# Kernel optimization log

Measured on AMD Instinct MI355X. Metric: run time of the kernel, lower is better.

The kernel has to match this reference:

```python
import jax, jax.numpy as jnp
import numpy as np

K = 3
P = K // 2


def _conv(x, w, b):
    y = jax.lax.conv_general_dilated(x, w, (1, 1), [(P, P), (P, P)],
                                     dimension_numbers=('NCHW', 'OIHW', 'NCHW'))
    return y + b[None, :, None, None]


def _deform_sample(x, py, px):
    # x: [B,C,H,W]; py,px: [B,KK,H,W] float sample coords -> [B,C,KK,H,W]
    B, C, H, W = x.shape
    xf = x.reshape(B, C, H * W)
    y0 = jnp.floor(py)
    x0 = jnp.floor(px)
    wy = py - y0
    wx = px - x0

    def corner(yi, xi, w):
        valid = (yi >= 0) & (yi < H) & (xi >= 0) & (xi < W)  # zero-pad outside
        idx = (jnp.clip(yi, 0, H - 1) * W + jnp.clip(xi, 0, W - 1)).astype(jnp.int32)
        g = jax.vmap(lambda xb, ib: xb[:, ib])(xf, idx)  # [B,C,KK,H,W]
        return g * (w * valid)[:, None]

    return (corner(y0, x0, (1 - wy) * (1 - wx)) + corner(y0, x0 + 1, (1 - wy) * wx)
            + corner(y0 + 1, x0, wy * (1 - wx)) + corner(y0 + 1, x0 + 1, wy * wx))


def setup_inputs() -> dict:
    key = jax.random.key(0)
    ks = jax.random.split(key, 8)
    B, C, H, W = 4, 256, 80, 80
    x = jax.random.normal(ks[0], (B, C, H, W), dtype=jnp.float32)
    offset_w = jax.random.normal(ks[1], (2 * K * K, C, K, K), dtype=jnp.float32) * 0.01
    offset_b = jax.random.normal(ks[2], (2 * K * K,), dtype=jnp.float32) * 0.01
    dcn_w = jax.random.normal(ks[3], (C, C, K, K), dtype=jnp.float32) * (1.0 / np.sqrt(C * K * K))
    gamma = jnp.ones((C,), jnp.float32)
    beta = jnp.zeros((C,), jnp.float32)
    mean = jax.random.normal(ks[4], (C,), dtype=jnp.float32) * 0.1
    var = jax.random.uniform(ks[5], (C,), dtype=jnp.float32, minval=0.5, maxval=1.5)
    return {'x': x, 'offset_w': offset_w, 'offset_b': offset_b, 'dcn_w': dcn_w,
            'gamma': gamma, 'beta': beta, 'mean': mean, 'var': var}


def reference(x, offset_w, offset_b, dcn_w, gamma, beta, mean, var):
    B, C, H, W = x.shape
    # offset conv -> [B, KK, 2(dy,dx), H, W] (torchvision DeformConv2d layout)
    off = _conv(x, offset_w, offset_b).reshape(B, K * K, 2, H, W)
    ki = jnp.repeat(jnp.arange(K), K).astype(x.dtype)  # kernel-tap row offset
    kj = jnp.tile(jnp.arange(K), K).astype(x.dtype)    # kernel-tap col offset
    hh = jnp.arange(H, dtype=x.dtype)
    ww = jnp.arange(W, dtype=x.dtype)
    py = off[:, :, 0] + (hh - P)[None, None, :, None] + ki[None, :, None, None]
    px = off[:, :, 1] + (ww - P)[None, None, None, :] + kj[None, :, None, None]
    vals = _deform_sample(x, py, px)                      # [B,C,KK,H,W]
    y = jnp.einsum('bckhw,ock->bohw', vals, dcn_w.reshape(C, C, K * K))
    # eval-mode BatchNorm + SiLU
    inv = jax.lax.rsqrt(var + 1e-5)
    y = (y - mean[None, :, None, None]) * (gamma * inv)[None, :, None, None] + beta[None, :, None, None]
    y = y * jax.nn.sigmoid(y)
    return x + y
```

## Files before the change

kernel.cpp:

```cpp
#include <hip/hip_runtime.h>
#include <math.h>
#include <stdint.h>

#define BATCH 4
#define CH    256
#define HH    80
#define WW    80
#define HW    (HH*WW)
#define NPIX  (BATCH*HW)
#define KK    9
#define CO    18
#define NCHUNK 72
#define NIV   36
#define PXB   64
#define NBLK  (NPIX/PXB)
#define AST   72

typedef _Float16 half8 __attribute__((ext_vector_type(8)));
typedef float    f32x4 __attribute__((ext_vector_type(4)));

__global__ __launch_bounds__(256) void k_transpose_x(const float* __restrict__ x,
                                                     _Float16* __restrict__ xt) {
    __shared__ float tile[32][33];
    int b  = blockIdx.z;
    int c0 = blockIdx.y * 32;
    int p0 = blockIdx.x * 32;
    int tx = threadIdx.x;
    int ty = threadIdx.y;
    const float* xb = x + (size_t)b * CH * HW;
    #pragma unroll
    for (int i = 0; i < 32; i += 8)
        tile[ty + i][tx] = xb[(size_t)(c0 + ty + i) * HW + p0 + tx];
    __syncthreads();
    _Float16* xtb = xt + (size_t)b * HW * CH;
    #pragma unroll
    for (int i = 0; i < 32; i += 8)
        xtb[(size_t)(p0 + ty + i) * CH + c0 + tx] = (_Float16)tile[tx][ty + i];
}

__global__ __launch_bounds__(256) void k_pack_all(const float* __restrict__ w,
                                                  const float* __restrict__ ow,
                                                  _Float16* __restrict__ wp,
                                                  _Float16* __restrict__ wpo) {
    int idx = blockIdx.x * 256 + threadIdx.x;
    if (idx < NIV * 16384) {
        int e    = idx & 7;
        int lane = (idx >> 3) & 63;
        int nn   = (idx >> 9) & 1;
        int ks   = (idx >> 10) & 1;
        int og   = (idx >> 11) & 7;
        int iv   = idx >> 14;
        int oc = og * 32 + nn * 16 + (lane & 15);
        int kl = ks * 32 + (lane >> 4) * 8 + e;
        int kg = iv * 64 + kl;
        int q  = kg >> 5;
        int tap = q >> 3;
        int c   = (q & 7) * 32 + (kg & 31);
        wp[idx] = (_Float16)w[((size_t)oc * CH + c) * KK + tap];
        return;
    }
    int idx2 = idx - NIV * 16384;
    if (idx2 >= NCHUNK * 1024) return;
    int e    = idx2 & 7;
    int lane = (idx2 >> 3) & 63;
    int nf   = (idx2 >> 9) & 1;
    int q    = idx2 >> 10;
    int oc  = nf * 16 + (lane & 15);
    int kic = (lane >> 4) * 8 + e;
    int tap = q >> 3;
    int c   = (q & 7) * 32 + kic;
    float v = (oc < CO) ? ow[((size_t)oc * CH + c) * KK + tap] : 0.f;
    wpo[idx2] = (_Float16)v;
}

__global__ __launch_bounds__(256) void k_offset(const _Float16* __restrict__ xt,
                                                const _Float16* __restrict__ wopf,
                                                float* __restrict__ off4) {
    int t = threadIdx.x, lane = t & 63, wvi = t >> 6;
    int lm = lane & 15, kg8 = (lane >> 4) * 8;
    int ksl = blockIdx.y;
    int pixbase = blockIdx.x * 64;
    int bb = pixbase / HW;
    int apx = pixbase % HW + wvi * 16 + lm;
    int h = apx / WW, w = apx % WW;
    const _Float16* xtb = xt + (size_t)bb * HW * CH;
    f32x4 acc0 = (f32x4)0.f, acc1 = (f32x4)0.f;
    #pragma unroll
    for (int qq = 0; qq < 18; ++qq) {
        int q = ksl * 18 + qq;
        int tap = q >> 3, cg = q & 7;
        int ki = tap / 3, kj = tap % 3;
        int yy = h + ki - 1, xx = w + kj - 1;
        bool ok = (yy >= 0) && (yy < HH) && (xx >= 0) && (xx < WW);
        int yc = min(max(yy, 0), HH - 1), xc = min(max(xx, 0), WW - 1);
        half8 a = {0, 0, 0, 0, 0, 0, 0, 0};
        if (ok) a = *(const half8*)(xtb + (size_t)(yc * WW + xc) * CH + cg * 32 + kg8);
        const _Float16* wb = wopf + (size_t)q * 1024 + lane * 8;
        half8 b0 = *(const half8*)(wb);
        half8 b1 = *(const half8*)(wb + 512);
        acc0 = __builtin_amdgcn_mfma_f32_16x16x32_f16(a, b0, acc0, 0, 0, 0);
        acc1 = __builtin_amdgcn_mfma_f32_16x16x32_f16(a, b1, acc1, 0, 0, 0);
    }
    float* op = off4 + (size_t)ksl * NPIX * CO;
    int prow = (lane >> 4) * 4;
    #pragma unroll
    for (int r = 0; r < 4; ++r) {
        int pix = pixbase + wvi * 16 + prow + r;
        op[(size_t)pix * CO + lm] = acc0[r];
        if (lm < CO - 16) op[(size_t)pix * CO + 16 + lm] = acc1[r];
    }
}

#define BODY(IV, BCUR, BNXT, RBUF, WBUF)                                           \
  {                                                                                \
    __syncthreads();                                                               \
    const int iv_ = (IV);                                                          \
    half8 pre[4]; float cwa[4];                                                    \
    if (iv_ < NIV - 1) {                                                           \
      const _Float16* wb = wpk4 + (size_t)(iv_ + 1) * 16384 + og * 2048 + lane * 8;\
      BNXT[0] = *(const half8*)(wb);                                               \
      BNXT[1] = *(const half8*)(wb + 512);                                         \
      BNXT[2] = *(const half8*)(wb + 1024);                                        \
      BNXT[3] = *(const half8*)(wb + 1536);                                        \
      int chunk = 2 * (iv_ + 1) + sub;                                             \
      int tap = chunk >> 3, cg = chunk & 7;                                        \
      int4 ncb = cbl[gpx][tap]; float4 ncw = cwl[gpx][tap];                        \
      pre[0] = *(const half8*)(xtb + (size_t)ncb.x + cg * 32 + ko);                \
      pre[1] = *(const half8*)(xtb + (size_t)ncb.y + cg * 32 + ko);                \
      pre[2] = *(const half8*)(xtb + (size_t)ncb.z + cg * 32 + ko);                \
      pre[3] = *(const half8*)(xtb + (size_t)ncb.w + cg * 32 + ko);                \
      cwa[0] = ncw.x; cwa[1] = ncw.y; cwa[2] = ncw.z; cwa[3] = ncw.w;              \
    }                                                                              \
    __builtin_amdgcn_s_setprio(1);                                                 \
    _Pragma("unroll")                                                              \
    for (int mm = 0; mm < 4; ++mm) {                                               \
      half8 a0 = *(const half8*)&Ab[RBUF][(mm * 16 + lm) * AST + kg8];             \
      half8 a1 = *(const half8*)&Ab[RBUF][(mm * 16 + lm) * AST + 32 + kg8];        \
      acc[mm][0] = __builtin_amdgcn_mfma_f32_16x16x32_f16(a0, BCUR[0], acc[mm][0], 0, 0, 0); \
      acc[mm][1] = __builtin_amdgcn_mfma_f32_16x16x32_f16(a0, BCUR[1], acc[mm][1], 0, 0, 0); \
      acc[mm][0] = __builtin_amdgcn_mfma_f32_16x16x32_f16(a1, BCUR[2], acc[mm][0], 0, 0, 0); \
      acc[mm][1] = __builtin_amdgcn_mfma_f32_16x16x32_f16(a1, BCUR[3], acc[mm][1], 0, 0, 0); \
    }                                                                              \
    __builtin_amdgcn_s_setprio(0);                                                 \
    if (iv_ < NIV - 1) {                                                           \
      half8 v = pre[0] * (_Float16)cwa[0];                                         \
      v += pre[1] * (_Float16)cwa[1];                                              \
      v += pre[2] * (_Float16)cwa[2];                                              \
      v += pre[3] * (_Float16)cwa[3];                                              \
      *(half8*)&Ab[WBUF][gpx * AST + cq * 8] = v;                                  \
    }                                                                              \
  }

__global__ __launch_bounds__(512, 4) void k_main(const float* __restrict__ x,
                                                 const _Float16* __restrict__ xt,
                                                 const _Float16* __restrict__ wpk4,
                                                 const float* __restrict__ off4,
                                                 const float* __restrict__ obias,
                                                 const float* __restrict__ gamma,
                                                 const float* __restrict__ beta,
                                                 const float* __restrict__ mean,
                                                 const float* __restrict__ var,
                                                 float* __restrict__ out) {
    __shared__ _Float16 Ab[2][PXB * AST];
    __shared__ int4     cbl[PXB][KK];
    __shared__ float4   cwl[PXB][KK];

    int t = threadIdx.x, lane = t & 63, og = t >> 6;
    int lm = lane & 15, kg8 = (lane >> 4) * 8;
    int tile = ((int)blockIdx.x & 7) * (NBLK / 8) + ((int)blockIdx.x >> 3);
    int pixbase = tile * PXB;
    int bb = pixbase / HW, hw0 = pixbase % HW;
    const _Float16* xtb = xt + (size_t)bb * HW * CH;

    for (int task = t; task < PXB * KK; task += 512) {
        int p = task / KK, tap = task - (task / KK) * KK;
        int pix = pixbase + p;
        float dy = obias[2 * tap], dx = obias[2 * tap + 1];
        #pragma unroll
        for (int ks = 0; ks < 4; ++ks) {
            dy += off4[(size_t)ks * NPIX * CO + (size_t)pix * CO + 2 * tap];
            dx += off4[(size_t)ks * NPIX * CO + (size_t)pix * CO + 2 * tap + 1];
        }
        int hw = pix % HW, hc = hw / WW, wc = hw % WW;
        int ki = tap / 3, kj = tap % 3;
        float py = dy + (float)(hc - 1 + ki);
        float px = dx + (float)(wc - 1 + kj);
        float y0f = floorf(py), x0f = floorf(px);
        float wy = py - y0f, wx = px - x0f;
        int y0 = (int)y0f, x0 = (int)x0f;
        int cb[4]; float cw[4];
        #pragma unroll
        for (int cy = 0; cy < 2; ++cy)
            #pragma unroll
            for (int cx = 0; cx < 2; ++cx) {
                int yy = y0 + cy, xx = x0 + cx;
                bool okc = (yy >= 0) && (yy < HH) && (xx >= 0) && (xx < WW);
                int yc = min(max(yy, 0), HH - 1);
                int xc = min(max(xx, 0), WW - 1);
                float wgt = (cy ? wy : 1.f - wy) * (cx ? wx : 1.f - wx);
                cb[cy * 2 + cx] = (yc * WW + xc) * CH;
                cw[cy * 2 + cx] = okc ? wgt : 0.f;
            }
        cbl[p][tap] = make_int4(cb[0], cb[1], cb[2], cb[3]);
        cwl[p][tap] = make_float4(cw[0], cw[1], cw[2], cw[3]);
    }
    __syncthreads();

    int gpx = t >> 3, cq = t & 7;
    int sub = cq >> 2, ko = (cq & 3) * 8;

    half8 bfA[4], bfB[4];
    {
        const _Float16* wb = wpk4 + og * 2048 + lane * 8;
        bfA[0] = *(const half8*)(wb);
        bfA[1] = *(const half8*)(wb + 512);
        bfA[2] = *(const half8*)(wb + 1024);
        bfA[3] = *(const half8*)(wb + 1536);
    }
    {
        int4 cb = cbl[gpx][0];
        float4 cw = cwl[gpx][0];
        int cg = sub;
        half8 v = *(const half8*)(xtb + (size_t)cb.x + cg * 32 + ko) * (_Float16)cw.x;
        v += *(const half8*)(xtb + (size_t)cb.y + cg * 32 + ko) * (_Float16)cw.y;
        v += *(const half8*)(xtb + (size_t)cb.z + cg * 32 + ko) * (_Float16)cw.z;
        v += *(const half8*)(xtb + (size_t)cb.w + cg * 32 + ko) * (_Float16)cw.w;
        *(half8*)&Ab[0][gpx * AST + cq * 8] = v;
    }

    f32x4 acc[4][2];
    #pragma unroll
    for (int mm = 0; mm < 4; ++mm) {
        acc[mm][0] = (f32x4)0.f;
        acc[mm][1] = (f32x4)0.f;
    }

    for (int ii = 0; ii < NIV; ii += 2) {
        BODY(ii,     bfA, bfB, 0, 1)
        BODY(ii + 1, bfB, bfA, 1, 0)
    }

    const float* xb2  = x   + (size_t)bb * CH * HW;
    float*       outb = out + (size_t)bb * CH * HW;
    #pragma unroll
    for (int nn = 0; nn < 2; ++nn) {
        int oc = og * 32 + nn * 16 + lm;
        float sc = gamma[oc] * rsqrtf(var[oc] + 1e-5f);
        float mn = mean[oc], bt = beta[oc];
        const float* xr   = xb2  + (size_t)oc * HW + hw0;
        float*       orow = outb + (size_t)oc * HW + hw0;
        #pragma unroll
        for (int mm = 0; mm < 4; ++mm) {
            int pb2 = mm * 16 + (lane >> 4) * 4;
            #pragma unroll
            for (int r = 0; r < 4; ++r) {
                float yv = (acc[mm][nn][r] - mn) * sc + bt;
                float s = yv * __builtin_amdgcn_rcpf(1.f + __expf(-yv));
                orow[pb2 + r] = xr[pb2 + r] + s;
            }
        }
    }
}

extern "C" void kernel_launch(void* const* d_in, const int* in_sizes, int n_in,
                              void* d_out, int out_size, void* d_ws, size_t ws_size,
                              hipStream_t stream) {
    const float* x        = (const float*)d_in[0];
    const float* offset_w = (const float*)d_in[1];
    const float* offset_b = (const float*)d_in[2];
    const float* dcn_w    = (const float*)d_in[3];
    const float* gamma    = (const float*)d_in[4];
    const float* beta     = (const float*)d_in[5];
    const float* mean     = (const float*)d_in[6];
    const float* var      = (const float*)d_in[7];
    float* out = (float*)d_out;

    _Float16* xt   = (_Float16*)d_ws;
    _Float16* wpk4 = xt + (size_t)NPIX * CH;
    _Float16* wopf = wpk4 + (size_t)NIV * 16384;
    float*    off4 = (float*)(wopf + (size_t)NCHUNK * 1024);

    k_transpose_x<<<dim3(HW / 32, CH / 32, BATCH), dim3(32, 8), 0, stream>>>(x, xt);
    k_pack_all<<<(NIV * 16384 + NCHUNK * 1024 + 255) / 256, 256, 0, stream>>>(dcn_w, offset_w, wpk4, wopf);
    k_offset<<<dim3(NBLK, 4), 256, 0, stream>>>(xt, wopf, off4);
    k_main<<<NBLK, 512, 0, stream>>>(x, xt, wpk4, off4, offset_b,
                                     gamma, beta, mean, var, out);
}
```

Baseline: 96.41 us.

## Split main GEMM reduction across two K-slices with fp16 partials and finish kernel

Splits the deformable GEMM's reduction dimension into two halves, run as separate blocks (grid y=2), so the launch has twice as many blocks and better fills the GPU. Each half writes fp16 partial sums to workspace, and a new elementwise kernel adds the halves and applies BatchNorm, SiLU and the residual. If the workspace is too small it falls back to the original fused kernel. The cost is an extra launch, extra global traffic for the partials and reduced precision from storing partials in fp16. Corner weights are now also computed twice, once per slice.

Measured after the change: 348.4 us. 261% more time.

```diff
diff --git a/kernel.cpp b/kernel.cpp
--- a/kernel.cpp
+++ b/kernel.cpp
@@ -17,6 +17,7 @@
 #define AST   72
 
 typedef _Float16 half8 __attribute__((ext_vector_type(8)));
+typedef _Float16 half4 __attribute__((ext_vector_type(4)));
 typedef float    f32x4 __attribute__((ext_vector_type(4)));
 
 __global__ __launch_bounds__(256) void k_transpose_x(const float* __restrict__ x,
@@ -111,68 +112,11 @@
     }
 }
 
-#define BODY(IV, BCUR, BNXT, RBUF, WBUF)                                           \
-  {                                                                                \
-    __syncthreads();                                                               \
-    const int iv_ = (IV);                                                          \
-    half8 pre[4]; float cwa[4];                                                    \
-    if (iv_ < NIV - 1) {                                                           \
-      const _Float16* wb = wpk4 + (size_t)(iv_ + 1) * 16384 + og * 2048 + lane * 8;\
-      BNXT[0] = *(const half8*)(wb);                                               \
-      BNXT[1] = *(const half8*)(wb + 512);                                         \
-      BNXT[2] = *(const half8*)(wb + 1024);                                        \
-      BNXT[3] = *(const half8*)(wb + 1536);                                        \
-      int chunk = 2 * (iv_ + 1) + sub;                                             \
-      int tap = chunk >> 3, cg = chunk & 7;                                        \
-      int4 ncb = cbl[gpx][tap]; float4 ncw = cwl[gpx][tap];                        \
-      pre[0] = *(const half8*)(xtb + (size_t)ncb.x + cg * 32 + ko);                \
-      pre[1] = *(const half8*)(xtb + (size_t)ncb.y + cg * 32 + ko);                \
-      pre[2] = *(const half8*)(xtb + (size_t)ncb.z + cg * 32 + ko);                \
-      pre[3] = *(const half8*)(xtb + (size_t)ncb.w + cg * 32 + ko);                \
-      cwa[0] = ncw.x; cwa[1] = ncw.y; cwa[2] = ncw.z; cwa[3] = ncw.w;              \
-    }                                                                              \
-    __builtin_amdgcn_s_setprio(1);                                                 \
-    _Pragma("unroll")                                                              \
-    for (int mm = 0; mm < 4; ++mm) {                                               \
-      half8 a0 = *(const half8*)&Ab[RBUF][(mm * 16 + lm) * AST + kg8];             \
-      half8 a1 = *(const half8*)&Ab[RBUF][(mm * 16 + lm) * AST + 32 + kg8];        \
-      acc[mm][0] = __builtin_amdgcn_mfma_f32_16x16x32_f16(a0, BCUR[0], acc[mm][0], 0, 0, 0); \
-      acc[mm][1] = __builtin_amdgcn_mfma_f32_16x16x32_f16(a0, BCUR[1], acc[mm][1], 0, 0, 0); \
-      acc[mm][0] = __builtin_amdgcn_mfma_f32_16x16x32_f16(a1, BCUR[2], acc[mm][0], 0, 0, 0); \
-      acc[mm][1] = __builtin_amdgcn_mfma_f32_16x16x32_f16(a1, BCUR[3], acc[mm][1], 0, 0, 0); \
-    }                                                                              \
-    __builtin_amdgcn_s_setprio(0);                                                 \
-    if (iv_ < NIV - 1) {                                                           \
-      half8 v = pre[0] * (_Float16)cwa[0];                                         \
-      v += pre[1] * (_Float16)cwa[1];                                              \
-      v += pre[2] * (_Float16)cwa[2];                                              \
-      v += pre[3] * (_Float16)cwa[3];                                              \
-      *(half8*)&Ab[WBUF][gpx * AST + cq * 8] = v;                                  \
-    }                                                                              \
-  }
-
-__global__ __launch_bounds__(512, 4) void k_main(const float* __restrict__ x,
-                                                 const _Float16* __restrict__ xt,
-                                                 const _Float16* __restrict__ wpk4,
-                                                 const float* __restrict__ off4,
-                                                 const float* __restrict__ obias,
-                                                 const float* __restrict__ gamma,
-                                                 const float* __restrict__ beta,
-                                                 const float* __restrict__ mean,
-                                                 const float* __restrict__ var,
-                                                 float* __restrict__ out) {
-    __shared__ _Float16 Ab[2][PXB * AST];
-    __shared__ int4     cbl[PXB][KK];
-    __shared__ float4   cwl[PXB][KK];
-
-    int t = threadIdx.x, lane = t & 63, og = t >> 6;
-    int lm = lane & 15, kg8 = (lane >> 4) * 8;
-    int tile = ((int)blockIdx.x & 7) * (NBLK / 8) + ((int)blockIdx.x >> 3);
-    int pixbase = tile * PXB;
-    int bb = pixbase / HW, hw0 = pixbase % HW;
-    const _Float16* xtb = xt + (size_t)bb * HW * CH;
-
-    for (int task = t; task < PXB * KK; task += 512) {
+__device__ __forceinline__ void build_corners(int t, int nthr, int pixbase,
+                                              const float* __restrict__ off4,
+                                              const float* __restrict__ obias,
+                                              int4 (*cbl)[KK], float4 (*cwl)[KK]) {
+    for (int task = t; task < PXB * KK; task += nthr) {
         int p = task / KK, tap = task - (task / KK) * KK;
         int pix = pixbase + p;
         float dy = obias[2 * tap], dx = obias[2 * tap + 1];
@@ -204,6 +148,171 @@
         cbl[p][tap] = make_int4(cb[0], cb[1], cb[2], cb[3]);
         cwl[p][tap] = make_float4(cw[0], cw[1], cw[2], cw[3]);
     }
+}
+
+#define BODY(IV, IVEND, BCUR, BNXT, RBUF, WBUF)                                    \
+  {                                                                                \
+    __syncthreads();                                                               \
+    const int iv_ = (IV);                                                          \
+    half8 pre[4]; float cwa[4];                                                    \
+    if (iv_ < (IVEND) - 1) {                                                       \
+      const _Float16* wb = wpk4 + (size_t)(iv_ + 1) * 16384 + og * 2048 + lane * 8;\
+      BNXT[0] = *(const half8*)(wb);                                               \
+      BNXT[1] = *(const half8*)(wb + 512);                                         \
+      BNXT[2] = *(const half8*)(wb + 1024);                                        \
+      BNXT[3] = *(const half8*)(wb + 1536);                                        \
+      int chunk = 2 * (iv_ + 1) + sub;                                             \
+      int tap = chunk >> 3, cg = chunk & 7;                                        \
+      int4 ncb = cbl[gpx][tap]; float4 ncw = cwl[gpx][tap];                        \
+      pre[0] = *(const half8*)(xtb + (size_t)ncb.x + cg * 32 + ko);                \
+      pre[1] = *(const half8*)(xtb + (size_t)ncb.y + cg * 32 + ko);                \
+      pre[2] = *(const half8*)(xtb + (size_t)ncb.z + cg * 32 + ko);                \
+      pre[3] = *(const half8*)(xtb + (size_t)ncb.w + cg * 32 + ko);                \
+      cwa[0] = ncw.x; cwa[1] = ncw.y; cwa[2] = ncw.z; cwa[3] = ncw.w;              \
+    }                                                                              \
+    __builtin_amdgcn_s_setprio(1);                                                 \
+    _Pragma("unroll")                                                              \
+    for (int mm = 0; mm < 4; ++mm) {                                               \
+      half8 a0 = *(const half8*)&Ab[RBUF][(mm * 16 + lm) * AST + kg8];             \
+      half8 a1 = *(const half8*)&Ab[RBUF][(mm * 16 + lm) * AST + 32 + kg8];        \
+      acc[mm][0] = __builtin_amdgcn_mfma_f32_16x16x32_f16(a0, BCUR[0], acc[mm][0], 0, 0, 0); \
+      acc[mm][1] = __builtin_amdgcn_mfma_f32_16x16x32_f16(a0, BCUR[1], acc[mm][1], 0, 0, 0); \
+      acc[mm][0] = __builtin_amdgcn_mfma_f32_16x16x32_f16(a1, BCUR[2], acc[mm][0], 0, 0, 0); \
+      acc[mm][1] = __builtin_amdgcn_mfma_f32_16x16x32_f16(a1, BCUR[3], acc[mm][1], 0, 0, 0); \
+    }                                                                              \
+    __builtin_amdgcn_s_setprio(0);                                                 \
+    if (iv_ < (IVEND) - 1) {                                                       \
+      half8 v = pre[0] * (_Float16)cwa[0];                                         \
+      v += pre[1] * (_Float16)cwa[1];                                              \
+      v += pre[2] * (_Float16)cwa[2];                                              \
+      v += pre[3] * (_Float16)cwa[3];                                              \
+      *(half8*)&Ab[WBUF][gpx * AST + cq * 8] = v;                                  \
+    }                                                                              \
+  }
+
+__global__ __launch_bounds__(512, 6) void k_main_sk(const _Float16* __restrict__ xt,
+                                                    const _Float16* __restrict__ wpk4,
+                                                    const float* __restrict__ off4,
+                                                    const float* __restrict__ obias,
+                                                    _Float16* __restrict__ P) {
+    __shared__ _Float16 Ab[2][PXB * AST];
+    __shared__ int4     cbl[PXB][KK];
+    __shared__ float4   cwl[PXB][KK];
+
+    int t = threadIdx.x, lane = t & 63, og = t >> 6;
+    int lm = lane & 15, kg8 = (lane >> 4) * 8;
+    int ksl = blockIdx.y;
+    int iv0 = ksl * (NIV / 2);
+    int tile = ((int)blockIdx.x & 7) * (NBLK / 8) + ((int)blockIdx.x >> 3);
+    int pixbase = tile * PXB;
+    int bb = pixbase / HW, hw0 = pixbase % HW;
+    const _Float16* xtb = xt + (size_t)bb * HW * CH;
+
+    build_corners(t, 512, pixbase, off4, obias, cbl, cwl);
+    __syncthreads();
+
+    int gpx = t >> 3, cq = t & 7;
+    int sub = cq >> 2, ko = (cq & 3) * 8;
+
+    half8 bfA[4], bfB[4];
+    {
+        const _Float16* wb = wpk4 + (size_t)iv0 * 16384 + og * 2048 + lane * 8;
+        bfA[0] = *(const half8*)(wb);
+        bfA[1] = *(const half8*)(wb + 512);
+        bfA[2] = *(const half8*)(wb + 1024);
+        bfA[3] = *(const half8*)(wb + 1536);
+    }
+    {
+        int chunk0 = 2 * iv0 + sub;
+        int tap0 = chunk0 >> 3, cg0 = chunk0 & 7;
+        int4 cb = cbl[gpx][tap0];
+        float4 cw = cwl[gpx][tap0];
+        half8 v = *(const half8*)(xtb + (size_t)cb.x + cg0 * 32 + ko) * (_Float16)cw.x;
+        v += *(const half8*)(xtb + (size_t)cb.y + cg0 * 32 + ko) * (_Float16)cw.y;
+        v += *(const half8*)(xtb + (size_t)cb.z + cg0 * 32 + ko) * (_Float16)cw.z;
+        v += *(const half8*)(xtb + (size_t)cb.w + cg0 * 32 + ko) * (_Float16)cw.w;
+        *(half8*)&Ab[0][gpx * AST + cq * 8] = v;
+    }
+
+    f32x4 acc[4][2];
+    #pragma unroll
+    for (int mm = 0; mm < 4; ++mm) {
+        acc[mm][0] = (f32x4)0.f;
+        acc[mm][1] = (f32x4)0.f;
+    }
+
+    int ivend = iv0 + NIV / 2;
+    for (int ii = iv0; ii < ivend; ii += 2) {
+        BODY(ii,     ivend, bfA, bfB, 0, 1)
+        BODY(ii + 1, ivend, bfB, bfA, 1, 0)
+    }
+
+    _Float16* Pb = P + (size_t)ksl * NPIX * CH + (size_t)bb * CH * HW;
+    #pragma unroll
+    for (int nn = 0; nn < 2; ++nn) {
+        int oc = og * 32 + nn * 16 + lm;
+        _Float16* prow = Pb + (size_t)oc * HW + hw0;
+        #pragma unroll
+        for (int mm = 0; mm < 4; ++mm) {
+            int pb2 = mm * 16 + (lane >> 4) * 4;
+            half4 h = {(_Float16)acc[mm][nn][0], (_Float16)acc[mm][nn][1],
+                       (_Float16)acc[mm][nn][2], (_Float16)acc[mm][nn][3]};
+            *(half4*)&prow[pb2] = h;
+        }
+    }
+}
+
+__global__ __launch_bounds__(512) void k_finish(const _Float16* __restrict__ P,
+                                                const float* __restrict__ x,
+                                                const float* __restrict__ gamma,
+                                                const float* __restrict__ beta,
+                                                const float* __restrict__ mean,
+                                                const float* __restrict__ var,
+                                                float* __restrict__ out) {
+    int tid = blockIdx.x * 512 + threadIdx.x;
+    size_t base = (size_t)tid * 8;
+    int oc = (tid / (HW / 8)) & (CH - 1);
+    half8 p0 = *(const half8*)(P + base);
+    half8 p1 = *(const half8*)(P + (size_t)NPIX * CH + base);
+    float sc = gamma[oc] * rsqrtf(var[oc] + 1e-5f);
+    float mn = mean[oc], bt = beta[oc];
+    float4 x0 = *(const float4*)(x + base);
+    float4 x1 = *(const float4*)(x + base + 4);
+    float o[8];
+    #pragma unroll
+    for (int j = 0; j < 8; ++j) {
+        float y = (float)p0[j] + (float)p1[j];
+        float yv = (y - mn) * sc + bt;
+        float s = yv * __builtin_amdgcn_rcpf(1.f + __expf(-yv));
+        float xv = (j < 4) ? ((const float*)&x0)[j] : ((const float*)&x1)[j - 4];
+        o[j] = xv + s;
+    }
+    *(float4*)(out + base)     = make_float4(o[0], o[1], o[2], o[3]);
+    *(float4*)(out + base + 4) = make_float4(o[4], o[5], o[6], o[7]);
+}
+
+__global__ __launch_bounds__(512, 4) void k_main_fused(const float* __restrict__ x,
+                                                       const _Float16* __restrict__ xt,
+                                                       const _Float16* __restrict__ wpk4,
+                                                       const float* __restrict__ off4,
+                                                       const float* __restrict__ obias,
+                                                       const float* __restrict__ gamma,
+                                                       const float* __restrict__ beta,
+                                                       const float* __restrict__ mean,
+                                                       const float* __restrict__ var,
+                                                       float* __restrict__ out) {
+    __shared__ _Float16 Ab[2][PXB * AST];
+    __shared__ int4     cbl[PXB][KK];
+    __shared__ float4   cwl[PXB][KK];
+
+    int t = threadIdx.x, lane = t & 63, og = t >> 6;
+    int lm = lane & 15, kg8 = (lane >> 4) * 8;
+    int tile = ((int)blockIdx.x & 7) * (NBLK / 8) + ((int)blockIdx.x >> 3);
+    int pixbase = tile * PXB;
+    int bb = pixbase / HW, hw0 = pixbase % HW;
+    const _Float16* xtb = xt + (size_t)bb * HW * CH;
+
+    build_corners(t, 512, pixbase, off4, obias, cbl, cwl);
     __syncthreads();
 
     int gpx = t >> 3, cq = t & 7;
@@ -236,8 +345,8 @@
     }
 
     for (int ii = 0; ii < NIV; ii += 2) {
-        BODY(ii,     bfA, bfB, 0, 1)
-        BODY(ii + 1, bfB, bfA, 1, 0)
+        BODY(ii,     NIV, bfA, bfB, 0, 1)
+        BODY(ii + 1, NIV, bfB, bfA, 1, 0)
     }
 
     const float* xb2  = x   + (size_t)bb * CH * HW;
@@ -279,10 +388,19 @@
     _Float16* wpk4 = xt + (size_t)NPIX * CH;
     _Float16* wopf = wpk4 + (size_t)NIV * 16384;
     float*    off4 = (float*)(wopf + (size_t)NCHUNK * 1024);
+    _Float16* P    = (_Float16*)(off4 + (size_t)4 * NPIX * CO);
+
+    const size_t NEED = 13107200ull + 1179648 + 147456 + 7372800 + 26214400;
 
     k_transpose_x<<<dim3(HW / 32, CH / 32, BATCH), dim3(32, 8), 0, stream>>>(x, xt);
     k_pack_all<<<(NIV * 16384 + NCHUNK * 1024 + 255) / 256, 256, 0, stream>>>(dcn_w, offset_w, wpk4, wopf);
     k_offset<<<dim3(NBLK, 4), 256, 0, stream>>>(xt, wopf, off4);
-    k_main<<<NBLK, 512, 0, stream>>>(x, xt, wpk4, off4, offset_b,
-                                     gamma, beta, mean, var, out);
-}
+
+    if (ws_size >= NEED) {
+        k_main_sk<<<dim3(NBLK, 2), 512, 0, stream>>>(xt, wpk4, off4, offset_b, P);
+        k_finish<<<(NPIX * CH / 8 + 511) / 512, 512, 0, stream>>>(P, x, gamma, beta, mean, var, out);
+    } else {
+        k_main_fused<<<NBLK, 512, 0, stream>>>(x, xt, wpk4, off4, offset_b,
+                                               gamma, beta, mean, var, out);
+    }
+}
```

## Shrink main tile to 32 pixels with 4 waves each owning 64 output channels

Applied to the files above, without the earlier changes.

The main deformable-conv GEMM kernel now handles 32 pixels per block with 256 threads. Each wave covers 64 output channels over 2 M-tiles, where before it covered 32 channels over 4 M-tiles. This doubles the number of blocks to improve load balance, and gives each A fragment more MFMA reuse. The explicit register double-buffering of B weights is dropped, so weights load each iteration without prefetch, and total weight traffic per pixel doubles because there are twice as many blocks. The offset-conv kernel's grid is pinned to 64-pixel tiles so it is unaffected by the PXB change.

Result: slower. 111.2 us (+15.3%).

```diff
diff --git a/kernel.cpp b/kernel.cpp
--- a/kernel.cpp
+++ b/kernel.cpp
@@ -12,7 +12,7 @@
 #define CO    18
 #define NCHUNK 72
 #define NIV   36
-#define PXB   64
+#define PXB   32
 #define NBLK  (NPIX/PXB)
 #define AST   72
 
@@ -111,47 +111,7 @@
     }
 }
 
-#define BODY(IV, BCUR, BNXT, RBUF, WBUF)                                           \
-  {                                                                                \
-    __syncthreads();                                                               \
-    const int iv_ = (IV);                                                          \
-    half8 pre[4]; float cwa[4];                                                    \
-    if (iv_ < NIV - 1) {                                                           \
-      const _Float16* wb = wpk4 + (size_t)(iv_ + 1) * 16384 + og * 2048 + lane * 8;\
-      BNXT[0] = *(const half8*)(wb);                                               \
-      BNXT[1] = *(const half8*)(wb + 512);                                         \
-      BNXT[2] = *(const half8*)(wb + 1024);                                        \
-      BNXT[3] = *(const half8*)(wb + 1536);                                        \
-      int chunk = 2 * (iv_ + 1) + sub;                                             \
-      int tap = chunk >> 3, cg = chunk & 7;                                        \
-      int4 ncb = cbl[gpx][tap]; float4 ncw = cwl[gpx][tap];                        \
-      pre[0] = *(const half8*)(xtb + (size_t)ncb.x + cg * 32 + ko);                \
-      pre[1] = *(const half8*)(xtb + (size_t)ncb.y + cg * 32 + ko);                \
-      pre[2] = *(const half8*)(xtb + (size_t)ncb.z + cg * 32 + ko);                \
-      pre[3] = *(const half8*)(xtb + (size_t)ncb.w + cg * 32 + ko);                \
-      cwa[0] = ncw.x; cwa[1] = ncw.y; cwa[2] = ncw.z; cwa[3] = ncw.w;              \
-    }                                                                              \
-    __builtin_amdgcn_s_setprio(1);                                                 \
-    _Pragma("unroll")                                                              \
-    for (int mm = 0; mm < 4; ++mm) {                                               \
-      half8 a0 = *(const half8*)&Ab[RBUF][(mm * 16 + lm) * AST + kg8];             \
-      half8 a1 = *(const half8*)&Ab[RBUF][(mm * 16 + lm) * AST + 32 + kg8];        \
-      acc[mm][0] = __builtin_amdgcn_mfma_f32_16x16x32_f16(a0, BCUR[0], acc[mm][0], 0, 0, 0); \
-      acc[mm][1] = __builtin_amdgcn_mfma_f32_16x16x32_f16(a0, BCUR[1], acc[mm][1], 0, 0, 0); \
-      acc[mm][0] = __builtin_amdgcn_mfma_f32_16x16x32_f16(a1, BCUR[2], acc[mm][0], 0, 0, 0); \
-      acc[mm][1] = __builtin_amdgcn_mfma_f32_16x16x32_f16(a1, BCUR[3], acc[mm][1], 0, 0, 0); \
-    }                                                                              \
-    __builtin_amdgcn_s_setprio(0);                                                 \
-    if (iv_ < NIV - 1) {                                                           \
-      half8 v = pre[0] * (_Float16)cwa[0];                                         \
-      v += pre[1] * (_Float16)cwa[1];                                              \
-      v += pre[2] * (_Float16)cwa[2];                                              \
-      v += pre[3] * (_Float16)cwa[3];                                              \
-      *(half8*)&Ab[WBUF][gpx * AST + cq * 8] = v;                                  \
-    }                                                                              \
-  }
-
-__global__ __launch_bounds__(512, 4) void k_main(const float* __restrict__ x,
+__global__ __launch_bounds__(256, 4) void k_main(const float* __restrict__ x,
                                                  const _Float16* __restrict__ xt,
                                                  const _Float16* __restrict__ wpk4,
                                                  const float* __restrict__ off4,
@@ -165,14 +125,14 @@
     __shared__ int4     cbl[PXB][KK];
     __shared__ float4   cwl[PXB][KK];
 
-    int t = threadIdx.x, lane = t & 63, og = t >> 6;
+    int t = threadIdx.x, lane = t & 63, wvi = t >> 6;
     int lm = lane & 15, kg8 = (lane >> 4) * 8;
     int tile = ((int)blockIdx.x & 7) * (NBLK / 8) + ((int)blockIdx.x >> 3);
     int pixbase = tile * PXB;
     int bb = pixbase / HW, hw0 = pixbase % HW;
     const _Float16* xtb = xt + (size_t)bb * HW * CH;
 
-    for (int task = t; task < PXB * KK; task += 512) {
+    for (int task = t; task < PXB * KK; task += 256) {
         int p = task / KK, tap = task - (task / KK) * KK;
         int pix = pixbase + p;
         float dy = obias[2 * tap], dx = obias[2 * tap + 1];
@@ -209,14 +169,6 @@
     int gpx = t >> 3, cq = t & 7;
     int sub = cq >> 2, ko = (cq & 3) * 8;
 
-    half8 bfA[4], bfB[4];
-    {
-        const _Float16* wb = wpk4 + og * 2048 + lane * 8;
-        bfA[0] = *(const half8*)(wb);
-        bfA[1] = *(const half8*)(wb + 512);
-        bfA[2] = *(const half8*)(wb + 1024);
-        bfA[3] = *(const half8*)(wb + 1536);
-    }
     {
         int4 cb = cbl[gpx][0];
         float4 cw = cwl[gpx][0];
@@ -228,29 +180,79 @@
         *(half8*)&Ab[0][gpx * AST + cq * 8] = v;
     }
 
-    f32x4 acc[4][2];
-    #pragma unroll
-    for (int mm = 0; mm < 4; ++mm) {
-        acc[mm][0] = (f32x4)0.f;
-        acc[mm][1] = (f32x4)0.f;
-    }
-
-    for (int ii = 0; ii < NIV; ii += 2) {
-        BODY(ii,     bfA, bfB, 0, 1)
-        BODY(ii + 1, bfB, bfA, 1, 0)
+    f32x4 acc[2][4];
+    #pragma unroll
+    for (int mm = 0; mm < 2; ++mm)
+        #pragma unroll
+        for (int nn = 0; nn < 4; ++nn) acc[mm][nn] = (f32x4)0.f;
+
+    for (int i = 0; i < NIV; ++i) {
+        int buf = i & 1;
+        __syncthreads();
+
+        half8 bf[2][4];
+        {
+            const _Float16* wb = wpk4 + (size_t)i * 16384 + (wvi * 2) * 2048 + lane * 8;
+            #pragma unroll
+            for (int og2 = 0; og2 < 2; ++og2)
+                #pragma unroll
+                for (int ks = 0; ks < 2; ++ks)
+                    #pragma unroll
+                    for (int nn = 0; nn < 2; ++nn)
+                        bf[ks][og2 * 2 + nn] = *(const half8*)(wb + og2 * 2048 + ks * 1024 + nn * 512);
+        }
+
+        half8 pre[4];
+        float cwa[4];
+        if (i < NIV - 1) {
+            int chunk = 2 * (i + 1) + sub;
+            int tap = chunk >> 3, cg = chunk & 7;
+            int4 ncb = cbl[gpx][tap];
+            float4 ncw = cwl[gpx][tap];
+            pre[0] = *(const half8*)(xtb + (size_t)ncb.x + cg * 32 + ko);
+            pre[1] = *(const half8*)(xtb + (size_t)ncb.y + cg * 32 + ko);
+            pre[2] = *(const half8*)(xtb + (size_t)ncb.z + cg * 32 + ko);
+            pre[3] = *(const half8*)(xtb + (size_t)ncb.w + cg * 32 + ko);
+            cwa[0] = ncw.x; cwa[1] = ncw.y; cwa[2] = ncw.z; cwa[3] = ncw.w;
+        }
+
+        half8 af[2][2];
+        #pragma unroll
+        for (int mm = 0; mm < 2; ++mm)
+            #pragma unroll
+            for (int ks = 0; ks < 2; ++ks)
+                af[mm][ks] = *(const half8*)&Ab[buf][(mm * 16 + lm) * AST + ks * 32 + kg8];
+
+        __builtin_amdgcn_s_setprio(1);
+        #pragma unroll
+        for (int ks = 0; ks < 2; ++ks)
+            #pragma unroll
+            for (int mm = 0; mm < 2; ++mm)
+                #pragma unroll
+                for (int nn = 0; nn < 4; ++nn)
+                    acc[mm][nn] = __builtin_amdgcn_mfma_f32_16x16x32_f16(af[mm][ks], bf[ks][nn], acc[mm][nn], 0, 0, 0);
+        __builtin_amdgcn_s_setprio(0);
+
+        if (i < NIV - 1) {
+            half8 v = pre[0] * (_Float16)cwa[0];
+            v += pre[1] * (_Float16)cwa[1];
+            v += pre[2] * (_Float16)cwa[2];
+            v += pre[3] * (_Float16)cwa[3];
+            *(half8*)&Ab[buf ^ 1][gpx * AST + cq * 8] = v;
+        }
     }
 
     const float* xb2  = x   + (size_t)bb * CH * HW;
     float*       outb = out + (size_t)bb * CH * HW;
     #pragma unroll
-    for (int nn = 0; nn < 2; ++nn) {
-        int oc = og * 32 + nn * 16 + lm;
+    for (int nn = 0; nn < 4; ++nn) {
+        int oc = wvi * 64 + nn * 16 + lm;
         float sc = gamma[oc] * rsqrtf(var[oc] + 1e-5f);
         float mn = mean[oc], bt = beta[oc];
         const float* xr   = xb2  + (size_t)oc * HW + hw0;
         float*       orow = outb + (size_t)oc * HW + hw0;
         #pragma unroll
-        for (int mm = 0; mm < 4; ++mm) {
+        for (int mm = 0; mm < 2; ++mm) {
             int pb2 = mm * 16 + (lane >> 4) * 4;
             #pragma unroll
             for (int r = 0; r < 4; ++r) {
@@ -282,7 +284,7 @@
 
     k_transpose_x<<<dim3(HW / 32, CH / 32, BATCH), dim3(32, 8), 0, stream>>>(x, xt);
     k_pack_all<<<(NIV * 16384 + NCHUNK * 1024 + 255) / 256, 256, 0, stream>>>(dcn_w, offset_w, wpk4, wopf);
-    k_offset<<<dim3(NBLK, 4), 256, 0, stream>>>(xt, wopf, off4);
-    k_main<<<NBLK, 512, 0, stream>>>(x, xt, wpk4, off4, offset_b,
+    k_offset<<<dim3(NPIX / 64, 4), 256, 0, stream>>>(xt, wopf, off4);
+    k_main<<<NBLK, 256, 0, stream>>>(x, xt, wpk4, off4, offset_b,
                                      gamma, beta, mean, var, out);
 }
```

## Fuse offset convolution into main deformable conv kernel via shared memory

Applied to the files above, without the earlier changes.

Removes the separate k_offset launch and its global off4 buffer. Each main-kernel block now computes the 18 offset channels for its own 64 pixels with MFMA, split across 8 waves (4 pixel groups × 2 K-halves), and stores the partial sums in shared memory before the sampling-coordinate stage. This drops one kernel launch and the global write/read round trip of the offset partials. In exchange every block does a serial prologue of 36 MFMA steps per wave and uses extra LDS, which may reduce occupancy.

New measurement: 91.92 us. 1.05x faster.

```diff
diff --git a/kernel.cpp b/kernel.cpp
--- a/kernel.cpp
+++ b/kernel.cpp
@@ -73,50 +73,12 @@
     wpo[idx2] = (_Float16)v;
 }
 
-__global__ __launch_bounds__(256) void k_offset(const _Float16* __restrict__ xt,
-                                                const _Float16* __restrict__ wopf,
-                                                float* __restrict__ off4) {
-    int t = threadIdx.x, lane = t & 63, wvi = t >> 6;
-    int lm = lane & 15, kg8 = (lane >> 4) * 8;
-    int ksl = blockIdx.y;
-    int pixbase = blockIdx.x * 64;
-    int bb = pixbase / HW;
-    int apx = pixbase % HW + wvi * 16 + lm;
-    int h = apx / WW, w = apx % WW;
-    const _Float16* xtb = xt + (size_t)bb * HW * CH;
-    f32x4 acc0 = (f32x4)0.f, acc1 = (f32x4)0.f;
-    #pragma unroll
-    for (int qq = 0; qq < 18; ++qq) {
-        int q = ksl * 18 + qq;
-        int tap = q >> 3, cg = q & 7;
-        int ki = tap / 3, kj = tap % 3;
-        int yy = h + ki - 1, xx = w + kj - 1;
-        bool ok = (yy >= 0) && (yy < HH) && (xx >= 0) && (xx < WW);
-        int yc = min(max(yy, 0), HH - 1), xc = min(max(xx, 0), WW - 1);
-        half8 a = {0, 0, 0, 0, 0, 0, 0, 0};
-        if (ok) a = *(const half8*)(xtb + (size_t)(yc * WW + xc) * CH + cg * 32 + kg8);
-        const _Float16* wb = wopf + (size_t)q * 1024 + lane * 8;
-        half8 b0 = *(const half8*)(wb);
-        half8 b1 = *(const half8*)(wb + 512);
-        acc0 = __builtin_amdgcn_mfma_f32_16x16x32_f16(a, b0, acc0, 0, 0, 0);
-        acc1 = __builtin_amdgcn_mfma_f32_16x16x32_f16(a, b1, acc1, 0, 0, 0);
-    }
-    float* op = off4 + (size_t)ksl * NPIX * CO;
-    int prow = (lane >> 4) * 4;
-    #pragma unroll
-    for (int r = 0; r < 4; ++r) {
-        int pix = pixbase + wvi * 16 + prow + r;
-        op[(size_t)pix * CO + lm] = acc0[r];
-        if (lm < CO - 16) op[(size_t)pix * CO + 16 + lm] = acc1[r];
-    }
-}
-
-#define BODY(IV, BCUR, BNXT, RBUF, WBUF)                                           \
+#define BODY(IV, IVEND, BCUR, BNXT, RBUF, WBUF)                                    \
   {                                                                                \
     __syncthreads();                                                               \
     const int iv_ = (IV);                                                          \
     half8 pre[4]; float cwa[4];                                                    \
-    if (iv_ < NIV - 1) {                                                           \
+    if (iv_ < (IVEND) - 1) {                                                       \
       const _Float16* wb = wpk4 + (size_t)(iv_ + 1) * 16384 + og * 2048 + lane * 8;\
       BNXT[0] = *(const half8*)(wb);                                               \
       BNXT[1] = *(const half8*)(wb + 512);                                         \
@@ -142,7 +104,7 @@
       acc[mm][1] = __builtin_amdgcn_mfma_f32_16x16x32_f16(a1, BCUR[3], acc[mm][1], 0, 0, 0); \
     }                                                                              \
     __builtin_amdgcn_s_setprio(0);                                                 \
-    if (iv_ < NIV - 1) {                                                           \
+    if (iv_ < (IVEND) - 1) {                                                       \
       half8 v = pre[0] * (_Float16)cwa[0];                                         \
       v += pre[1] * (_Float16)cwa[1];                                              \
       v += pre[2] * (_Float16)cwa[2];                                              \
@@ -154,7 +116,7 @@
 __global__ __launch_bounds__(512, 4) void k_main(const float* __restrict__ x,
                                                  const _Float16* __restrict__ xt,
                                                  const _Float16* __restrict__ wpk4,
-                                                 const float* __restrict__ off4,
+                                                 const _Float16* __restrict__ wopf,
                                                  const float* __restrict__ obias,
                                                  const float* __restrict__ gamma,
                                                  const float* __restrict__ beta,
@@ -164,6 +126,7 @@
     __shared__ _Float16 Ab[2][PXB * AST];
     __shared__ int4     cbl[PXB][KK];
     __shared__ float4   cwl[PXB][KK];
+    __shared__ float    offl[2][PXB][CO];
 
     int t = threadIdx.x, lane = t & 63, og = t >> 6;
     int lm = lane & 15, kg8 = (lane >> 4) * 8;
@@ -172,17 +135,43 @@
     int bb = pixbase / HW, hw0 = pixbase % HW;
     const _Float16* xtb = xt + (size_t)bb * HW * CH;
 
+    {
+        int pxf = og & 3, kh = og >> 2;
+        int apx = hw0 + pxf * 16 + lm;
+        int h = apx / WW, w = apx % WW;
+        f32x4 oacc0 = (f32x4)0.f, oacc1 = (f32x4)0.f;
+        #pragma unroll
+        for (int qq = 0; qq < NCHUNK / 2; ++qq) {
+            int q = kh * (NCHUNK / 2) + qq;
+            int tap = q >> 3, cg = q & 7;
+            int ki = tap / 3, kj = tap - ki * 3;
+            int yy = h + ki - 1, xx = w + kj - 1;
+            bool ok = (yy >= 0) && (yy < HH) && (xx >= 0) && (xx < WW);
+            int yc = min(max(yy, 0), HH - 1), xc = min(max(xx, 0), WW - 1);
+            half8 a = {0, 0, 0, 0, 0, 0, 0, 0};
+            if (ok) a = *(const half8*)(xtb + (size_t)(yc * WW + xc) * CH + cg * 32 + kg8);
+            const _Float16* wb = wopf + (size_t)q * 1024 + lane * 8;
+            half8 b0 = *(const half8*)(wb);
+            half8 b1 = *(const half8*)(wb + 512);
+            oacc0 = __builtin_amdgcn_mfma_f32_16x16x32_f16(a, b0, oacc0, 0, 0, 0);
+            oacc1 = __builtin_amdgcn_mfma_f32_16x16x32_f16(a, b1, oacc1, 0, 0, 0);
+        }
+        int prow = pxf * 16 + (lane >> 4) * 4;
+        #pragma unroll
+        for (int r = 0; r < 4; ++r) offl[kh][prow + r][lm] = oacc0[r];
+        if (lm < CO - 16) {
+            #pragma unroll
+            for (int r = 0; r < 4; ++r) offl[kh][prow + r][16 + lm] = oacc1[r];
+        }
+    }
+    __syncthreads();
+
     for (int task = t; task < PXB * KK; task += 512) {
         int p = task / KK, tap = task - (task / KK) * KK;
-        int pix = pixbase + p;
-        float dy = obias[2 * tap], dx = obias[2 * tap + 1];
-        #pragma unroll
-        for (int ks = 0; ks < 4; ++ks) {
-            dy += off4[(size_t)ks * NPIX * CO + (size_t)pix * CO + 2 * tap];
-            dx += off4[(size_t)ks * NPIX * CO + (size_t)pix * CO + 2 * tap + 1];
-        }
-        int hw = pix % HW, hc = hw / WW, wc = hw % WW;
-        int ki = tap / 3, kj = tap % 3;
+        float dy = offl[0][p][2 * tap]     + offl[1][p][2 * tap]     + obias[2 * tap];
+        float dx = offl[0][p][2 * tap + 1] + offl[1][p][2 * tap + 1] + obias[2 * tap + 1];
+        int hw = hw0 + p, hc = hw / WW, wc = hw % WW;
+        int ki = tap / 3, kj = tap - ki * 3;
         float py = dy + (float)(hc - 1 + ki);
         float px = dx + (float)(wc - 1 + kj);
         float y0f = floorf(py), x0f = floorf(px);
@@ -236,8 +225,8 @@
     }
 
     for (int ii = 0; ii < NIV; ii += 2) {
-        BODY(ii,     bfA, bfB, 0, 1)
-        BODY(ii + 1, bfB, bfA, 1, 0)
+        BODY(ii,     NIV, bfA, bfB, 0, 1)
+        BODY(ii + 1, NIV, bfB, bfA, 1, 0)
     }
 
     const float* xb2  = x   + (size_t)bb * CH * HW;
@@ -278,11 +267,9 @@
     _Float16* xt   = (_Float16*)d_ws;
     _Float16* wpk4 = xt + (size_t)NPIX * CH;
     _Float16* wopf = wpk4 + (size_t)NIV * 16384;
-    float*    off4 = (float*)(wopf + (size_t)NCHUNK * 1024);
 
     k_transpose_x<<<dim3(HW / 32, CH / 32, BATCH), dim3(32, 8), 0, stream>>>(x, xt);
     k_pack_all<<<(NIV * 16384 + NCHUNK * 1024 + 255) / 256, 256, 0, stream>>>(dcn_w, offset_w, wpk4, wopf);
-    k_offset<<<dim3(NBLK, 4), 256, 0, stream>>>(xt, wopf, off4);
-    k_main<<<NBLK, 512, 0, stream>>>(x, xt, wpk4, off4, offset_b,
+    k_main<<<NBLK, 512, 0, stream>>>(x, xt, wpk4, wopf, offset_b,
                                      gamma, beta, mean, var, out);
 }
```
